# Kernel optimization log

Hardware: AMD Instinct MI355X
Metric: run time of the kernel (lower is better)

## Reference

```python
import jax, jax.numpy as jnp
import numpy as np

B, N, D, H, DK, MS, FF = 8, 256, 256, 16, 16, 16, 512
EPS = 1e-5


def _inorm(x, scale, bias):
    # InstanceNorm1d over the node dim (axis=1) per channel, affine
    m = jnp.mean(x, axis=1, keepdims=True)
    v = jnp.var(x, axis=1, keepdims=True)
    return (x - m) * jax.lax.rsqrt(v + EPS) * scale + bias


def _heads(x):
    b, n, _ = x.shape
    return x.reshape(b, n, H, DK).transpose(0, 2, 1, 3)  # (b,H,n,DK)


def _block(emb_r, emb_c, cost, Wq, Wk, Wv, m1w, m1b, m2w, m2b, cw, cb,
           n1s, n1b, w1, b1, w2, b2, n2s, n2b):
    b, n, _ = emb_r.shape
    q = _heads(emb_r @ Wq)
    k = _heads(emb_c @ Wk)
    v = _heads(emb_c @ Wv)
    dot = jnp.einsum('bhid,bhjd->bhij', q, k) / jnp.sqrt(jnp.float32(DK))
    # stack dot-product score with cost-matrix score: (b,H,r,c,2)
    two = jnp.stack([dot, jnp.broadcast_to(cost[:, None], dot.shape)], axis=-1)
    # per-head 2 -> MS -> 1 MLP on each (row,col) score pair
    ms1 = jax.nn.relu(jnp.einsum('bhrcs,hsm->bhrcm', two, m1w)
                      + m1b[None, :, None, None, :])
    mixed = jnp.einsum('bhrcm,hm->bhrc', ms1, m2w[:, :, 0]) \
            + m2b[:, 0][None, :, None, None]
    w = jax.nn.softmax(mixed, axis=-1)
    out = jnp.einsum('bhrc,bhcd->bhrd', w, v)
    out_concat = out.transpose(0, 2, 1, 3).reshape(b, n, H * DK)
    mh = out_concat @ cw + cb
    out1 = _inorm(emb_r + mh, n1s, n1b)
    ff = jax.nn.relu(out1 @ w1 + b1) @ w2 + b2
    return _inorm(out1 + ff, n2s, n2b)


def setup_inputs() -> dict:
    key = jax.random.key(0)
    keys = iter(jax.random.split(key, 64))
    def nrm(shape, s=0.05):
        return jax.random.normal(next(keys), shape, dtype=jnp.float32) * s
    inp = {
        'row_emb': nrm((B, N, D), 1.0),
        'col_emb': nrm((B, N, D), 1.0),
        'cost_mat': jax.random.uniform(next(keys), (B, N, N), dtype=jnp.float32),
    }
    for p in ('r', 'c'):
        inp[p + 'Wq'] = nrm((D, H * DK)); inp[p + 'Wk'] = nrm((D, H * DK)); inp[p + 'Wv'] = nrm((D, H * DK))
        inp[p + 'm1w'] = nrm((H, 2, MS), 0.5); inp[p + 'm1b'] = nrm((H, MS), 0.5)
        inp[p + 'm2w'] = nrm((H, MS, 1), 0.25); inp[p + 'm2b'] = nrm((H, 1), 0.25)
        inp[p + 'cw'] = nrm((H * DK, D)); inp[p + 'cb'] = jnp.zeros((D,), jnp.float32)
        inp[p + 'n1s'] = jnp.ones((D,), jnp.float32); inp[p + 'n1b'] = jnp.zeros((D,), jnp.float32)
        inp[p + 'w1'] = nrm((D, FF)); inp[p + 'b1'] = jnp.zeros((FF,), jnp.float32)
        inp[p + 'w2'] = nrm((FF, D)); inp[p + 'b2'] = jnp.zeros((D,), jnp.float32)
        inp[p + 'n2s'] = jnp.ones((D,), jnp.float32); inp[p + 'n2b'] = jnp.zeros((D,), jnp.float32)
    return inp


def reference(row_emb, col_emb, cost_mat,
              rWq, rWk, rWv, rm1w, rm1b, rm2w, rm2b, rcw, rcb,
              rn1s, rn1b, rw1, rb1, rw2, rb2, rn2s, rn2b,
              cWq, cWk, cWv, cm1w, cm1b, cm2w, cm2b, ccw, ccb,
              cn1s, cn1b, cw1, cb1, cw2, cb2, cn2s, cn2b):
    row_out = _block(row_emb, col_emb, cost_mat,
                     rWq, rWk, rWv, rm1w, rm1b, rm2w, rm2b, rcw, rcb,
                     rn1s, rn1b, rw1, rb1, rw2, rb2, rn2s, rn2b)
    col_out = _block(col_emb, row_emb, cost_mat.transpose(0, 2, 1),
                     cWq, cWk, cWv, cm1w, cm1b, cm2w, cm2b, ccw, ccb,
                     cn1s, cn1b, cw1, cb1, cw2, cb2, cn2s, cn2b)
    return row_out, col_out
```

## Files before the change

kernel.cpp:

```cpp
#include <hip/hip_runtime.h>
#include <hip/hip_bf16.h>
#include <hip/hip_fp16.h>

#define Bc 8
#define Nc 256
#define Dc 256
#define Hc 16
#define DKc 16
#define MSc 16
#define FFc 512
#define SZc 524288
#define WHALF 524288
#define FFH 1048576

typedef __hip_bfloat16 bf16;
typedef __attribute__((ext_vector_type(8))) short bfrag8;
typedef __attribute__((ext_vector_type(4))) float f32x4;

__device__ __forceinline__ short f2bs(float x) {
    bf16 t = __float2bfloat16(x);
    return *reinterpret_cast<short*>(&t);
}

__device__ __forceinline__ __half2 pk_relu(__half2 x) {
    __half2 r;
    asm("v_pk_max_f16 %0, %1, 0" : "=v"(r) : "v"(x));
    return r;
}

__global__ void setup_kernel(const float* __restrict__ e0, const float* __restrict__ e1,
                             bf16* __restrict__ o0, bf16* __restrict__ o1,
                             float* __restrict__ statsB,
                             const float* rWq, const float* rWk, const float* rWv,
                             const float* rcw, const float* rw1, const float* rw2,
                             const float* cWq, const float* cWk, const float* cWv,
                             const float* ccw, const float* cw1, const float* cw2,
                             bf16* __restrict__ WT) {
    int y = blockIdx.y;
    if (y < 2) {
        const float* src = y ? e1 : e0;
        bf16* dst = y ? o1 : o0;
        size_t base = (size_t)blockIdx.x * 2048 + threadIdx.x;
#pragma unroll
        for (int i = 0; i < 8; ++i)
            dst[base + i * 256] = __float2bfloat16(src[base + i * 256]);
        return;
    }
    if (y == 2) {
        if (blockIdx.x < 64) statsB[blockIdx.x * 256 + threadIdx.x] = 0.f;
        return;
    }
    int z = y - 3;
    int p = z / 6, widx = z % 6;
    const float* src; int K, N; size_t off;
    switch (widx) {
        case 0: src = p ? cWq : rWq; K = 256; N = 256; off = 0; break;
        case 1: src = p ? cWk : rWk; K = 256; N = 256; off = 65536; break;
        case 2: src = p ? cWv : rWv; K = 256; N = 256; off = 131072; break;
        case 3: src = p ? ccw : rcw; K = 256; N = 256; off = 196608; break;
        case 4: src = p ? cw1 : rw1; K = 256; N = 512; off = 262144; break;
        default: src = p ? cw2 : rw2; K = 512; N = 256; off = 393216; break;
    }
    int Ntiles = N >> 5, Ktiles = K >> 5;
    if ((int)blockIdx.x >= Ktiles * Ntiles) return;
    int kt = blockIdx.x / Ntiles, nt = blockIdx.x - kt * Ntiles;
    int k0 = kt * 32, n0 = nt * 32;
    bf16* dst = WT + (size_t)p * WHALF + off;
    __shared__ float t[32][33];
    int tx = threadIdx.x & 31, ty = threadIdx.x >> 5;
#pragma unroll
    for (int i = 0; i < 4; ++i)
        t[ty + i * 8][tx] = src[(size_t)(k0 + ty + i * 8) * N + n0 + tx];
    __syncthreads();
#pragma unroll
    for (int i = 0; i < 4; ++i)
        dst[(size_t)(n0 + ty + i * 8) * K + k0 + tx] = __float2bfloat16(t[tx][ty + i * 8]);
}

__device__ __forceinline__ void mfma_loop(const short* pa0, const short* pa1,
                                          const short* pb, int K,
                                          f32x4& acc0, f32x4& acc1) {
    for (int kt = 0; kt < K; kt += 32) {
        bfrag8 a0 = *(const bfrag8*)(pa0 + kt);
        bfrag8 a1 = *(const bfrag8*)(pa1 + kt);
        bfrag8 b  = *(const bfrag8*)(pb + kt);
        acc0 = __builtin_amdgcn_mfma_f32_16x16x32_bf16(a0, b, acc0, 0, 0, 0);
        acc1 = __builtin_amdgcn_mfma_f32_16x16x32_bf16(a1, b, acc1, 0, 0, 0);
    }
}

__global__ void gemm_qkv_kernel(const short* __restrict__ embRb, const short* __restrict__ embCb,
                                const short* __restrict__ WT, float* __restrict__ qkv) {
    int z = blockIdx.z;
    int p = z / 3, j = z % 3;
    const short* A  = (j == 0) ? (p ? embCb : embRb) : (p ? embRb : embCb);
    const short* BT = WT + (size_t)p * WHALF + j * 65536;
    float* out = qkv + (size_t)z * SZc;

    int lane = threadIdx.x & 63, w = threadIdx.x >> 6;
    int m_base = blockIdx.x * 64 + (w & 1) * 32;
    int n_base = blockIdx.y * 32 + (w >> 1) * 16;
    int mr = lane & 15, quad = lane >> 4;

    const short* pa0 = A + (size_t)(m_base + mr) * 256 + quad * 8;
    const short* pa1 = pa0 + 16 * 256;
    const short* pb  = BT + (size_t)(n_base + mr) * 256 + quad * 8;

    f32x4 acc0 = {0.f, 0.f, 0.f, 0.f}, acc1 = {0.f, 0.f, 0.f, 0.f};
    mfma_loop(pa0, pa1, pb, 256, acc0, acc1);

    int col = n_base + mr;
    int h = col >> 4, dk = col & 15;
#pragma unroll
    for (int r = 0; r < 4; ++r) {
        int row0 = m_base + quad * 4 + r;
        int row1 = row0 + 16;
        int b0 = row0 >> 8, n0 = row0 & 255;
        int b1 = row1 >> 8, n1 = row1 & 255;
        out[((size_t)(b0 * Hc + h) * Nc + n0) * DKc + dk] = acc0[r];
        out[((size_t)(b1 * Hc + h) * Nc + n1) * DKc + dk] = acc1[r];
    }
}

__global__ void attn_kernel(const float* __restrict__ qkv, const float* __restrict__ cost,
                            const float* rm1w, const float* rm1b,
                            const float* rm2w, const float* rm2b,
                            const float* cm1w, const float* cm1b,
                            const float* cm2w, const float* cm2b,
                            bf16* __restrict__ attnb) {
    int b = blockIdx.x, h = blockIdx.y;
    int p = blockIdx.z >> 4, rc = blockIdx.z & 15;
    const float* Q = qkv + (size_t)(p * 3 + 0) * SZc;
    const float* K = qkv + (size_t)(p * 3 + 1) * SZc;
    const float* V = qkv + (size_t)(p * 3 + 2) * SZc;
    const float* m1w = p ? cm1w : rm1w;
    const float* m1b = p ? cm1b : rm1b;
    const float* m2w = p ? cm2w : rm2w;
    const float* m2b = p ? cm2b : rm2b;
    bf16* out_concat = attnb + (size_t)p * SZc;

    int bh = b * Hc + h;
    int r0 = rc * 16;
    int c = threadIdx.x;
    int lane = c & 63, wid = c >> 6;
    int mr = lane & 15, quad = lane >> 4;

    __shared__ __align__(16) short sVT[16 * 264];
    __shared__ __align__(16) short sEb[16 * 264];
    __shared__ float sPart[4 * 256];
    __shared__ float sSum[16 * 4];
    __shared__ __half2 sWd[16], sWc[16], sWb[16], sW2[16];
    __shared__ float sm2bS[1];

    {
        const float* vp = V + ((size_t)bh * Nc + c) * DKc;
#pragma unroll
        for (int i = 0; i < 4; ++i) {
            float4 vv = *(const float4*)(vp + i * 4);
            sVT[(i * 4 + 0) * 264 + c] = f2bs(vv.x);
            sVT[(i * 4 + 1) * 264 + c] = f2bs(vv.y);
            sVT[(i * 4 + 2) * 264 + c] = f2bs(vv.z);
            sVT[(i * 4 + 3) * 264 + c] = f2bs(vv.w);
        }
    }
    if (c >= 64 && c < 80) {
        int m = c - 64;
        sWd[m] = __float2half2_rn(m1w[h * 32 + m] * 0.25f);
        sWc[m] = __float2half2_rn(m1w[h * 32 + 16 + m]);
        sWb[m] = __float2half2_rn(m1b[h * 16 + m]);
        sW2[m] = __float2half2_rn(m2w[h * 16 + m]);
    } else if (c == 128) sm2bS[0] = m2b[h];

    bfrag8 qf = {0, 0, 0, 0, 0, 0, 0, 0};
    if (quad < 2) {
        const float* qp = Q + ((size_t)bh * Nc + r0 + mr) * DKc + quad * 8;
        float4 qa = *(const float4*)qp;
        float4 qb = *(const float4*)(qp + 4);
        qf[0] = f2bs(qa.x); qf[1] = f2bs(qa.y); qf[2] = f2bs(qa.z); qf[3] = f2bs(qa.w);
        qf[4] = f2bs(qb.x); qf[5] = f2bs(qb.y); qf[6] = f2bs(qb.z); qf[7] = f2bs(qb.w);
    }

    __half2 sv2[8];
#pragma unroll
    for (int t = 0; t < 4; ++t) {
        bfrag8 kf = {0, 0, 0, 0, 0, 0, 0, 0};
        if (quad < 2) {
            const float* kp = K + ((size_t)bh * Nc + wid * 64 + t * 16 + mr) * DKc + quad * 8;
            float4 ka = *(const float4*)kp;
            float4 kb = *(const float4*)(kp + 4);
            kf[0] = f2bs(ka.x); kf[1] = f2bs(ka.y); kf[2] = f2bs(ka.z); kf[3] = f2bs(ka.w);
            kf[4] = f2bs(kb.x); kf[5] = f2bs(kb.y); kf[6] = f2bs(kb.z); kf[7] = f2bs(kb.w);
        }
        f32x4 acc = {0.f, 0.f, 0.f, 0.f};
        acc = __builtin_amdgcn_mfma_f32_16x16x32_bf16(qf, kf, acc, 0, 0, 0);
        sv2[t * 2]     = __floats2half2_rn(acc[0], acc[1]);
        sv2[t * 2 + 1] = __floats2half2_rn(acc[2], acc[3]);
    }

    const float* costR = cost + (size_t)b * Nc * Nc;
    __half2 cv2[8];
    if (p) {
#pragma unroll
        for (int t = 0; t < 4; ++t) {
            float4 cvv = *(const float4*)(costR +
                (size_t)(wid * 64 + t * 16 + mr) * Nc + r0 + quad * 4);
            cv2[t * 2]     = __floats2half2_rn(cvv.x, cvv.y);
            cv2[t * 2 + 1] = __floats2half2_rn(cvv.z, cvv.w);
        }
    } else {
#pragma unroll
        for (int t = 0; t < 4; ++t) {
            float c0 = costR[(size_t)(r0 + quad * 4 + 0) * Nc + wid * 64 + t * 16 + mr];
            float c1 = costR[(size_t)(r0 + quad * 4 + 1) * Nc + wid * 64 + t * 16 + mr];
            float c2 = costR[(size_t)(r0 + quad * 4 + 2) * Nc + wid * 64 + t * 16 + mr];
            float c3 = costR[(size_t)(r0 + quad * 4 + 3) * Nc + wid * 64 + t * 16 + mr];
            cv2[t * 2]     = __floats2half2_rn(c0, c1);
            cv2[t * 2 + 1] = __floats2half2_rn(c2, c3);
        }
    }

    __syncthreads();

    const __half2 z2 = __half2half2(__float2half(0.f));
    __half2 mix2[8] = {z2, z2, z2, z2, z2, z2, z2, z2};
    for (int m = 0; m < MSc; ++m) {
        __half2 w1d = sWd[m];
        __half2 w1c = sWc[m];
        __half2 b1v = sWb[m];
        __half2 w2v = sW2[m];
#pragma unroll
        for (int s = 0; s < 8; ++s) {
            __half2 tt = __hfma2(sv2[s], w1d, __hfma2(cv2[s], w1c, b1v));
            mix2[s] = __hfma2(pk_relu(tt), w2v, mix2[s]);
        }
    }
    float b2v = sm2bS[0];
    float ex[16];
#pragma unroll
    for (int s = 0; s < 8; ++s) {
        float2 mf = __half22float2(mix2[s]);
        ex[s * 2]     = __expf(mf.x + b2v);
        ex[s * 2 + 1] = __expf(mf.y + b2v);
    }

#pragma unroll
    for (int t = 0; t < 4; ++t)
#pragma unroll
        for (int r = 0; r < 4; ++r)
            sEb[(quad * 4 + r) * 264 + wid * 64 + t * 16 + mr] = f2bs(ex[t * 4 + r]);

#pragma unroll
    for (int r = 0; r < 4; ++r) {
        float rp = ex[r] + ex[4 + r] + ex[8 + r] + ex[12 + r];
        rp += __shfl_xor(rp, 1);
        rp += __shfl_xor(rp, 2);
        rp += __shfl_xor(rp, 4);
        rp += __shfl_xor(rp, 8);
        if (mr == 0) sSum[(quad * 4 + r) * 4 + wid] = rp;
    }
    __syncthreads();

    {
        const short* pa = &sEb[mr * 264 + wid * 64 + quad * 8];
        const short* pb = &sVT[mr * 264 + wid * 64 + quad * 8];
        f32x4 acc = {0.f, 0.f, 0.f, 0.f};
        bfrag8 a0 = *(const bfrag8*)pa;
        bfrag8 b0 = *(const bfrag8*)pb;
        acc = __builtin_amdgcn_mfma_f32_16x16x32_bf16(a0, b0, acc, 0, 0, 0);
        bfrag8 a1 = *(const bfrag8*)(pa + 32);
        bfrag8 b1 = *(const bfrag8*)(pb + 32);
        acc = __builtin_amdgcn_mfma_f32_16x16x32_bf16(a1, b1, acc, 0, 0, 0);
#pragma unroll
        for (int r = 0; r < 4; ++r)
            sPart[wid * 256 + (quad * 4 + r) * 16 + mr] = acc[r];
    }
    __syncthreads();

    {
        int r = c >> 4, dk = c & 15;
        float o = sPart[c] + sPart[256 + c] + sPart[512 + c] + sPart[768 + c];
        float sum = sSum[r * 4] + sSum[r * 4 + 1] + sSum[r * 4 + 2] + sSum[r * 4 + 3];
        out_concat[((size_t)(b * Nc + r0 + r)) * Dc + h * DKc + dk] =
            __float2bfloat16(o / sum);
    }
}

__global__ void gemm_cat_kernel(const short* __restrict__ attnb, const short* __restrict__ WT,
                                const float* rcb, const float* ccb,
                                const float* __restrict__ resR, const float* __restrict__ resC,
                                float* __restrict__ x1, float* __restrict__ stats1) {
    int p = blockIdx.z;
    const short* A  = attnb + (size_t)p * SZc;
    const short* BT = WT + (size_t)p * WHALF + 196608;
    const float* bias = p ? ccb : rcb;
    const float* res  = p ? resC : resR;
    float* outF = x1 + (size_t)p * SZc;
    float* st   = stats1 + p * 4096;

    int lane = threadIdx.x & 63, w = threadIdx.x >> 6;
    int m_base = blockIdx.x * 64 + (w & 1) * 32;
    int n_base = blockIdx.y * 32 + (w >> 1) * 16;
    int mr = lane & 15, quad = lane >> 4;

    const short* pa0 = A + (size_t)(m_base + mr) * 256 + quad * 8;
    const short* pa1 = pa0 + (size_t)16 * 256;
    const short* pb  = BT + (size_t)(n_base + mr) * 256 + quad * 8;

    f32x4 acc0 = {0.f, 0.f, 0.f, 0.f}, acc1 = {0.f, 0.f, 0.f, 0.f};
    mfma_loop(pa0, pa1, pb, 256, acc0, acc1);

    int col = n_base + mr;
    float bv = bias[col];
    int bb = m_base >> 8;
    float ssum = 0.f, ssq = 0.f;
#pragma unroll
    for (int r = 0; r < 4; ++r) {
        int row0 = m_base + quad * 4 + r;
        int row1 = row0 + 16;
        float v0 = acc0[r] + bv + res[(size_t)row0 * 256 + col];
        float v1 = acc1[r] + bv + res[(size_t)row1 * 256 + col];
        outF[(size_t)row0 * 256 + col] = v0;
        outF[(size_t)row1 * 256 + col] = v1;
        ssum += v0 + v1;
        ssq  += v0 * v0 + v1 * v1;
    }
    atomicAdd(&st[(bb * 256 + col) * 2],     ssum);
    atomicAdd(&st[(bb * 256 + col) * 2 + 1], ssq);
}

__global__ __launch_bounds__(256) void gemm_ff1n_kernel(
        const float* __restrict__ x1, const float* __restrict__ stats1,
        const float* rn1s, const float* rn1b, const float* cn1s, const float* cn1b,
        const short* __restrict__ WT, const float* rb1, const float* cb1,
        bf16* __restrict__ ffh) {
    int p = blockIdx.z;
    const float* X   = x1 + (size_t)p * SZc;
    const float* st  = stats1 + p * 4096;
    const float* n1s = p ? cn1s : rn1s;
    const float* n1b = p ? cn1b : rn1b;
    const short* BT  = WT + (size_t)p * WHALF + 262144;
    const float* bias = p ? cb1 : rb1;
    bf16* outB = ffh + (size_t)p * FFH;

    __shared__ __align__(16) short sA[64 * 264];
    int c = threadIdx.x;
    int m_base = blockIdx.x * 64;
    int b = m_base >> 8;

    float s = st[(b * 256 + c) * 2];
    float q = st[(b * 256 + c) * 2 + 1];
    float mean = s * (1.f / Nc);
    float var = q * (1.f / Nc) - mean * mean;
    float inv = rsqrtf(var + 1e-5f) * n1s[c];
    float nb = n1b[c];
#pragma unroll 8
    for (int i = 0; i < 64; ++i) {
        float v = X[(size_t)(m_base + i) * 256 + c];
        sA[i * 264 + c] = f2bs((v - mean) * inv + nb);
    }
    __syncthreads();

    int lane = c & 63, w = c >> 6;
    int mloc = (w & 1) * 32;
    int n_base = blockIdx.y * 32 + (w >> 1) * 16;
    int mr = lane & 15, quad = lane >> 4;

    const short* pa0 = &sA[(mloc + mr) * 264 + quad * 8];
    const short* pa1 = pa0 + 16 * 264;
    const short* pb  = BT + (size_t)(n_base + mr) * 256 + quad * 8;

    f32x4 acc0 = {0.f, 0.f, 0.f, 0.f}, acc1 = {0.f, 0.f, 0.f, 0.f};
#pragma unroll
    for (int kt = 0; kt < 256; kt += 32) {
        bfrag8 a0 = *(const bfrag8*)(pa0 + kt);
        bfrag8 a1 = *(const bfrag8*)(pa1 + kt);
        bfrag8 bb = *(const bfrag8*)(pb + kt);
        acc0 = __builtin_amdgcn_mfma_f32_16x16x32_bf16(a0, bb, acc0, 0, 0, 0);
        acc1 = __builtin_amdgcn_mfma_f32_16x16x32_bf16(a1, bb, acc1, 0, 0, 0);
    }

    int col = n_base + mr;
    float bv = bias[col];
#pragma unroll
    for (int r = 0; r < 4; ++r) {
        int row0 = m_base + mloc + quad * 4 + r;
        int row1 = row0 + 16;
        outB[(size_t)row0 * 512 + col] = __float2bfloat16(fmaxf(acc0[r] + bv, 0.f));
        outB[(size_t)row1 * 512 + col] = __float2bfloat16(fmaxf(acc1[r] + bv, 0.f));
    }
}

__global__ void gemm_ff2n_kernel(const short* __restrict__ ffh, const short* __restrict__ WT,
                                 const float* rb2, const float* cb2,
                                 const float* __restrict__ x1, const float* __restrict__ stats1,
                                 const float* rn1s, const float* rn1b,
                                 const float* cn1s, const float* cn1b,
                                 float* __restrict__ ff2, float* __restrict__ stats2) {
    int p = blockIdx.z;
    const short* A  = ffh + (size_t)p * FFH;
    const short* BT = WT + (size_t)p * WHALF + 393216;
    const float* bias = p ? cb2 : rb2;
    const float* X   = x1 + (size_t)p * SZc;
    const float* st1 = stats1 + p * 4096;
    const float* n1s = p ? cn1s : rn1s;
    const float* n1b = p ? cn1b : rn1b;
    float* outF = ff2 + (size_t)p * SZc;
    float* st2  = stats2 + p * 4096;

    int lane = threadIdx.x & 63, w = threadIdx.x >> 6;
    int m_base = blockIdx.x * 64 + (w & 1) * 32;
    int n_base = blockIdx.y * 32 + (w >> 1) * 16;
    int mr = lane & 15, quad = lane >> 4;

    const short* pa0 = A + (size_t)(m_base + mr) * 512 + quad * 8;
    const short* pa1 = pa0 + (size_t)16 * 512;
    const short* pb  = BT + (size_t)(n_base + mr) * 512 + quad * 8;

    f32x4 acc0 = {0.f, 0.f, 0.f, 0.f}, acc1 = {0.f, 0.f, 0.f, 0.f};
    mfma_loop(pa0, pa1, pb, 512, acc0, acc1);

    int col = n_base + mr;
    int bb = m_base >> 8;
    float s1 = st1[(bb * 256 + col) * 2];
    float q1 = st1[(bb * 256 + col) * 2 + 1];
    float mean1 = s1 * (1.f / Nc);
    float var1 = q1 * (1.f / Nc) - mean1 * mean1;
    float inv1 = rsqrtf(var1 + 1e-5f) * n1s[col];
    float nb1 = n1b[col];
    float bv = bias[col];

    float ssum = 0.f, ssq = 0.f;
#pragma unroll
    for (int r = 0; r < 4; ++r) {
        int row0 = m_base + quad * 4 + r;
        int row1 = row0 + 16;
        float res0 = (X[(size_t)row0 * 256 + col] - mean1) * inv1 + nb1;
        float res1 = (X[(size_t)row1 * 256 + col] - mean1) * inv1 + nb1;
        float v0 = acc0[r] + bv + res0;
        float v1 = acc1[r] + bv + res1;
        outF[(size_t)row0 * 256 + col] = v0;
        outF[(size_t)row1 * 256 + col] = v1;
        ssum += v0 + v1;
        ssq  += v0 * v0 + v1 * v1;
    }
    atomicAdd(&st2[(bb * 256 + col) * 2],     ssum);
    atomicAdd(&st2[(bb * 256 + col) * 2 + 1], ssq);
}

__global__ void apply_kernel(const float* __restrict__ x, const float* __restrict__ stats,
                             const float* sR, const float* bR,
                             const float* sC, const float* bC,
                             float* __restrict__ outF) {
    int p = blockIdx.y;
    int row = blockIdx.x;
    int b = row >> 8;
    int d = threadIdx.x;
    const float* st = stats + p * 4096;
    float sum = st[(b * 256 + d) * 2];
    float sq  = st[(b * 256 + d) * 2 + 1];
    float mean = sum * (1.f / Nc);
    float var = sq * (1.f / Nc) - mean * mean;
    float inv = rsqrtf(var + 1e-5f);
    float scale = (p ? sC : sR)[d];
    float bias  = (p ? bC : bR)[d];
    float v = x[(size_t)p * SZc + (size_t)row * Dc + d];
    outF[(size_t)p * SZc + (size_t)row * Dc + d] = (v - mean) * inv * scale + bias;
}

extern "C" void kernel_launch(void* const* d_in, const int* in_sizes, int n_in,
                              void* d_out, int out_size, void* d_ws, size_t ws_size,
                              hipStream_t stream) {
    const float* row_emb = (const float*)d_in[0];
    const float* col_emb = (const float*)d_in[1];
    const float* cost    = (const float*)d_in[2];
    float* out = (float*)d_out;
    float* ws = (float*)d_ws;
#define RP(i) ((const float*)d_in[3 + (i)])
#define CP(i) ((const float*)d_in[20 + (i)])

    float* qkv    = ws;
    float* x1     = ws + 6 * (size_t)SZc;
    float* ff2    = ws + 8 * (size_t)SZc;
    float* statsB = ws + 10 * (size_t)SZc;
    bf16* bfbase  = (bf16*)(statsB + 16384);
    bf16* embRb = bfbase;
    bf16* embCb = embRb + SZc;
    bf16* attnb = embCb + SZc;
    bf16* ffh   = attnb + 2 * (size_t)SZc;
    bf16* WT    = ffh + 4 * (size_t)SZc;
    float* stats1 = statsB;
    float* stats2 = statsB + 8192;

    setup_kernel<<<dim3(256, 15), 256, 0, stream>>>(
        row_emb, col_emb, embRb, embCb, statsB,
        RP(0), RP(1), RP(2), RP(7), RP(11), RP(13),
        CP(0), CP(1), CP(2), CP(7), CP(11), CP(13), WT);
    gemm_qkv_kernel<<<dim3(32, 8, 6), 256, 0, stream>>>(
        (const short*)embRb, (const short*)embCb, (const short*)WT, qkv);
    attn_kernel<<<dim3(Bc, Hc, 32), 256, 0, stream>>>(
        qkv, cost, RP(3), RP(4), RP(5), RP(6), CP(3), CP(4), CP(5), CP(6), attnb);
    gemm_cat_kernel<<<dim3(32, 8, 2), 256, 0, stream>>>(
        (const short*)attnb, (const short*)WT, RP(8), CP(8), row_emb, col_emb, x1, stats1);
    gemm_ff1n_kernel<<<dim3(32, 16, 2), 256, 0, stream>>>(
        x1, stats1, RP(9), RP(10), CP(9), CP(10),
        (const short*)WT, RP(12), CP(12), ffh);
    gemm_ff2n_kernel<<<dim3(32, 8, 2), 256, 0, stream>>>(
        (const short*)ffh, (const short*)WT, RP(14), CP(14),
        x1, stats1, RP(9), RP(10), CP(9), CP(10), ff2, stats2);
    apply_kernel<<<dim3(2048, 2), 256, 0, stream>>>(
        ff2, stats2, RP(15), RP(16), CP(15), CP(16), out);
#undef RP
#undef CP
}
```

Baseline: 230.4 us.

## Store QKV in bf16, prepack MLP weights in setup, vectorize norm apply

The QKV projection now writes bf16 instead of fp32. The attention kernel therefore loads Q, K and V as packed bf16 fragments directly, which halves that traffic and removes per-load conversions. The per-head score-MLP weights are converted to half2 once in the setup kernel and read from global memory in a fully unrolled loop, replacing the per-block shared-memory staging. The final instance-norm apply kernel is vectorized to float4 with four rows per block. Q, K and V were already rounded to bf16 before the MFMA, so precision is essentially unchanged.

```diff
diff --git a/kernel.cpp b/kernel.cpp
--- a/kernel.cpp
+++ b/kernel.cpp
@@ -35,6 +35,9 @@
                              const float* rcw, const float* rw1, const float* rw2,
                              const float* cWq, const float* cWk, const float* cWv,
                              const float* ccw, const float* cw1, const float* cw2,
+                             const float* rm1w, const float* rm1b, const float* rm2w,
+                             const float* cm1w, const float* cm1b, const float* cm2w,
+                             __half2* __restrict__ Wpk,
                              bf16* __restrict__ WT) {
     int y = blockIdx.y;
     if (y < 2) {
@@ -47,7 +50,20 @@
         return;
     }
     if (y == 2) {
-        if (blockIdx.x < 64) statsB[blockIdx.x * 256 + threadIdx.x] = 0.f;
+        if (blockIdx.x < 64) {
+            statsB[blockIdx.x * 256 + threadIdx.x] = 0.f;
+        } else if (blockIdx.x < 66) {
+            int p = blockIdx.x - 64;
+            const float* m1w = p ? cm1w : rm1w;
+            const float* m1b = p ? cm1b : rm1b;
+            const float* m2w = p ? cm2w : rm2w;
+            int h = threadIdx.x >> 4, m = threadIdx.x & 15;
+            __half2* wp = Wpk + (size_t)(p * 16 + h) * 64;
+            wp[m]      = __float2half2_rn(m1w[h * 32 + m] * 0.25f);
+            wp[16 + m] = __float2half2_rn(m1w[h * 32 + 16 + m]);
+            wp[32 + m] = __float2half2_rn(m1b[h * 16 + m]);
+            wp[48 + m] = __float2half2_rn(m2w[h * 16 + m]);
+        }
         return;
     }
     int z = y - 3;
@@ -90,12 +106,12 @@
 }
 
 __global__ void gemm_qkv_kernel(const short* __restrict__ embRb, const short* __restrict__ embCb,
-                                const short* __restrict__ WT, float* __restrict__ qkv) {
+                                const short* __restrict__ WT, bf16* __restrict__ qkv) {
     int z = blockIdx.z;
     int p = z / 3, j = z % 3;
     const short* A  = (j == 0) ? (p ? embCb : embRb) : (p ? embRb : embCb);
     const short* BT = WT + (size_t)p * WHALF + j * 65536;
-    float* out = qkv + (size_t)z * SZc;
+    bf16* out = qkv + (size_t)z * SZc;
 
     int lane = threadIdx.x & 63, w = threadIdx.x >> 6;
     int m_base = blockIdx.x * 64 + (w & 1) * 32;
@@ -117,26 +133,22 @@
         int row1 = row0 + 16;
         int b0 = row0 >> 8, n0 = row0 & 255;
         int b1 = row1 >> 8, n1 = row1 & 255;
-        out[((size_t)(b0 * Hc + h) * Nc + n0) * DKc + dk] = acc0[r];
-        out[((size_t)(b1 * Hc + h) * Nc + n1) * DKc + dk] = acc1[r];
-    }
-}
-
-__global__ void attn_kernel(const float* __restrict__ qkv, const float* __restrict__ cost,
-                            const float* rm1w, const float* rm1b,
-                            const float* rm2w, const float* rm2b,
-                            const float* cm1w, const float* cm1b,
-                            const float* cm2w, const float* cm2b,
+        out[((size_t)(b0 * Hc + h) * Nc + n0) * DKc + dk] = __float2bfloat16(acc0[r]);
+        out[((size_t)(b1 * Hc + h) * Nc + n1) * DKc + dk] = __float2bfloat16(acc1[r]);
+    }
+}
+
+__global__ void attn_kernel(const short* __restrict__ qkv, const float* __restrict__ cost,
+                            const __half2* __restrict__ Wpk,
+                            const float* rm2b, const float* cm2b,
                             bf16* __restrict__ attnb) {
     int b = blockIdx.x, h = blockIdx.y;
     int p = blockIdx.z >> 4, rc = blockIdx.z & 15;
-    const float* Q = qkv + (size_t)(p * 3 + 0) * SZc;
-    const float* K = qkv + (size_t)(p * 3 + 1) * SZc;
-    const float* V = qkv + (size_t)(p * 3 + 2) * SZc;
-    const float* m1w = p ? cm1w : rm1w;
-    const float* m1b = p ? cm1b : rm1b;
-    const float* m2w = p ? cm2w : rm2w;
-    const float* m2b = p ? cm2b : rm2b;
+    const short* Q = qkv + (size_t)(p * 3 + 0) * SZc;
+    const short* K = qkv + (size_t)(p * 3 + 1) * SZc;
+    const short* V = qkv + (size_t)(p * 3 + 2) * SZc;
+    const __half2* wp = Wpk + (size_t)(p * 16 + h) * 64;
+    float b2v = (p ? cm2b : rm2b)[h];
     bf16* out_concat = attnb + (size_t)p * SZc;
 
     int bh = b * Hc + h;
@@ -149,48 +161,28 @@
     __shared__ __align__(16) short sEb[16 * 264];
     __shared__ float sPart[4 * 256];
     __shared__ float sSum[16 * 4];
-    __shared__ __half2 sWd[16], sWc[16], sWb[16], sW2[16];
-    __shared__ float sm2bS[1];
 
     {
-        const float* vp = V + ((size_t)bh * Nc + c) * DKc;
-#pragma unroll
-        for (int i = 0; i < 4; ++i) {
-            float4 vv = *(const float4*)(vp + i * 4);
-            sVT[(i * 4 + 0) * 264 + c] = f2bs(vv.x);
-            sVT[(i * 4 + 1) * 264 + c] = f2bs(vv.y);
-            sVT[(i * 4 + 2) * 264 + c] = f2bs(vv.z);
-            sVT[(i * 4 + 3) * 264 + c] = f2bs(vv.w);
+        const short* vp = V + ((size_t)bh * Nc + c) * DKc;
+        bfrag8 v0 = *(const bfrag8*)vp;
+        bfrag8 v1 = *(const bfrag8*)(vp + 8);
+#pragma unroll
+        for (int i = 0; i < 8; ++i) {
+            sVT[i * 264 + c]       = v0[i];
+            sVT[(8 + i) * 264 + c] = v1[i];
         }
     }
-    if (c >= 64 && c < 80) {
-        int m = c - 64;
-        sWd[m] = __float2half2_rn(m1w[h * 32 + m] * 0.25f);
-        sWc[m] = __float2half2_rn(m1w[h * 32 + 16 + m]);
-        sWb[m] = __float2half2_rn(m1b[h * 16 + m]);
-        sW2[m] = __float2half2_rn(m2w[h * 16 + m]);
-    } else if (c == 128) sm2bS[0] = m2b[h];
 
     bfrag8 qf = {0, 0, 0, 0, 0, 0, 0, 0};
-    if (quad < 2) {
-        const float* qp = Q + ((size_t)bh * Nc + r0 + mr) * DKc + quad * 8;
-        float4 qa = *(const float4*)qp;
-        float4 qb = *(const float4*)(qp + 4);
-        qf[0] = f2bs(qa.x); qf[1] = f2bs(qa.y); qf[2] = f2bs(qa.z); qf[3] = f2bs(qa.w);
-        qf[4] = f2bs(qb.x); qf[5] = f2bs(qb.y); qf[6] = f2bs(qb.z); qf[7] = f2bs(qb.w);
-    }
+    if (quad < 2)
+        qf = *(const bfrag8*)(Q + ((size_t)bh * Nc + r0 + mr) * DKc + quad * 8);
 
     __half2 sv2[8];
 #pragma unroll
     for (int t = 0; t < 4; ++t) {
         bfrag8 kf = {0, 0, 0, 0, 0, 0, 0, 0};
-        if (quad < 2) {
-            const float* kp = K + ((size_t)bh * Nc + wid * 64 + t * 16 + mr) * DKc + quad * 8;
-            float4 ka = *(const float4*)kp;
-            float4 kb = *(const float4*)(kp + 4);
-            kf[0] = f2bs(ka.x); kf[1] = f2bs(ka.y); kf[2] = f2bs(ka.z); kf[3] = f2bs(ka.w);
-            kf[4] = f2bs(kb.x); kf[5] = f2bs(kb.y); kf[6] = f2bs(kb.z); kf[7] = f2bs(kb.w);
-        }
+        if (quad < 2)
+            kf = *(const bfrag8*)(K + ((size_t)bh * Nc + wid * 64 + t * 16 + mr) * DKc + quad * 8);
         f32x4 acc = {0.f, 0.f, 0.f, 0.f};
         acc = __builtin_amdgcn_mfma_f32_16x16x32_bf16(qf, kf, acc, 0, 0, 0);
         sv2[t * 2]     = __floats2half2_rn(acc[0], acc[1]);
@@ -223,18 +215,18 @@
 
     const __half2 z2 = __half2half2(__float2half(0.f));
     __half2 mix2[8] = {z2, z2, z2, z2, z2, z2, z2, z2};
+#pragma unroll
     for (int m = 0; m < MSc; ++m) {
-        __half2 w1d = sWd[m];
-        __half2 w1c = sWc[m];
-        __half2 b1v = sWb[m];
-        __half2 w2v = sW2[m];
+        __half2 w1d = wp[m];
+        __half2 w1c = wp[16 + m];
+        __half2 b1v = wp[32 + m];
+        __half2 w2v = wp[48 + m];
 #pragma unroll
         for (int s = 0; s < 8; ++s) {
             __half2 tt = __hfma2(sv2[s], w1d, __hfma2(cv2[s], w1c, b1v));
             mix2[s] = __hfma2(pk_relu(tt), w2v, mix2[s]);
         }
     }
-    float b2v = sm2bS[0];
     float ex[16];
 #pragma unroll
     for (int s = 0; s < 8; ++s) {
@@ -452,19 +444,32 @@
                              const float* sC, const float* bC,
                              float* __restrict__ outF) {
     int p = blockIdx.y;
-    int row = blockIdx.x;
+    int t = threadIdx.x;
+    int row = blockIdx.x * 4 + (t >> 6);
+    int d0 = (t & 63) * 4;
     int b = row >> 8;
-    int d = threadIdx.x;
-    const float* st = stats + p * 4096;
-    float sum = st[(b * 256 + d) * 2];
-    float sq  = st[(b * 256 + d) * 2 + 1];
-    float mean = sum * (1.f / Nc);
-    float var = sq * (1.f / Nc) - mean * mean;
-    float inv = rsqrtf(var + 1e-5f);
-    float scale = (p ? sC : sR)[d];
-    float bias  = (p ? bC : bR)[d];
-    float v = x[(size_t)p * SZc + (size_t)row * Dc + d];
-    outF[(size_t)p * SZc + (size_t)row * Dc + d] = (v - mean) * inv * scale + bias;
+    const float* st = stats + p * 4096 + (size_t)(b * 256 + d0) * 2;
+    float4 s01 = *(const float4*)st;
+    float4 s23 = *(const float4*)(st + 4);
+    const float* sp = p ? sC : sR;
+    const float* bp = p ? bC : bR;
+    float4 sc = *(const float4*)(sp + d0);
+    float4 bi = *(const float4*)(bp + d0);
+    float4 v = *(const float4*)(x + (size_t)p * SZc + (size_t)row * Dc + d0);
+    float sums[4] = {s01.x, s01.z, s23.x, s23.z};
+    float sqs[4]  = {s01.y, s01.w, s23.y, s23.w};
+    float vv[4]   = {v.x, v.y, v.z, v.w};
+    float scs[4]  = {sc.x, sc.y, sc.z, sc.w};
+    float bis[4]  = {bi.x, bi.y, bi.z, bi.w};
+    float4 o;
+#pragma unroll
+    for (int j = 0; j < 4; ++j) {
+        float mean = sums[j] * (1.f / Nc);
+        float var = sqs[j] * (1.f / Nc) - mean * mean;
+        float inv = rsqrtf(var + 1e-5f);
+        ((float*)&o)[j] = (vv[j] - mean) * inv * scs[j] + bis[j];
+    }
+    *(float4*)(outF + (size_t)p * SZc + (size_t)row * Dc + d0) = o;
 }
 
 extern "C" void kernel_launch(void* const* d_in, const int* in_sizes, int n_in,
@@ -478,12 +483,13 @@
 #define RP(i) ((const float*)d_in[3 + (i)])
 #define CP(i) ((const float*)d_in[20 + (i)])
 
-    float* qkv    = ws;
-    float* x1     = ws + 6 * (size_t)SZc;
-    float* ff2    = ws + 8 * (size_t)SZc;
-    float* statsB = ws + 10 * (size_t)SZc;
-    bf16* bfbase  = (bf16*)(statsB + 16384);
-    bf16* embRb = bfbase;
+    float* x1     = ws;
+    float* ff2    = ws + 2 * (size_t)SZc;
+    float* statsB = ws + 4 * (size_t)SZc;
+    __half2* Wpk  = (__half2*)(statsB + 16384);
+    bf16* bfbase  = (bf16*)(Wpk + 4096);
+    bf16* qkvb  = bfbase;
+    bf16* embRb = qkvb + 6 * (size_t)SZc;
     bf16* embCb = embRb + SZc;
     bf16* attnb = embCb + SZc;
     bf16* ffh   = attnb + 2 * (size_t)SZc;
@@ -494,11 +500,12 @@
     setup_kernel<<<dim3(256, 15), 256, 0, stream>>>(
         row_emb, col_emb, embRb, embCb, statsB,
         RP(0), RP(1), RP(2), RP(7), RP(11), RP(13),
-        CP(0), CP(1), CP(2), CP(7), CP(11), CP(13), WT);
+        CP(0), CP(1), CP(2), CP(7), CP(11), CP(13),
+        RP(3), RP(4), RP(5), CP(3), CP(4), CP(5), Wpk, WT);
     gemm_qkv_kernel<<<dim3(32, 8, 6), 256, 0, stream>>>(
-        (const short*)embRb, (const short*)embCb, (const short*)WT, qkv);
+        (const short*)embRb, (const short*)embCb, (const short*)WT, qkvb);
     attn_kernel<<<dim3(Bc, Hc, 32), 256, 0, stream>>>(
-        qkv, cost, RP(3), RP(4), RP(5), RP(6), CP(3), CP(4), CP(5), CP(6), attnb);
+        (const short*)qkvb, cost, Wpk, RP(6), CP(6), attnb);
     gemm_cat_kernel<<<dim3(32, 8, 2), 256, 0, stream>>>(
         (const short*)attnb, (const short*)WT, RP(8), CP(8), row_emb, col_emb, x1, stats1);
     gemm_ff1n_kernel<<<dim3(32, 16, 2), 256, 0, stream>>>(
@@ -507,7 +514,7 @@
     gemm_ff2n_kernel<<<dim3(32, 8, 2), 256, 0, stream>>>(
         (const short*)ffh, (const short*)WT, RP(14), CP(14),
         x1, stats1, RP(9), RP(10), CP(9), CP(10), ff2, stats2);
-    apply_kernel<<<dim3(2048, 2), 256, 0, stream>>>(
+    apply_kernel<<<dim3(512, 2), 256, 0, stream>>>(
         ff2, stats2, RP(15), RP(16), CP(15), CP(16), out);
 #undef RP
 #undef CP
```

Measured after the change: 216.4 us. 6.1% less time.
